# Kernel optimization log

Measured on AMD Instinct MI355X. Metric: run time of the kernel, lower is better.

## Reference

```python
import jax, jax.numpy as jnp
import numpy as np

BASE_RES = 192          # image_shape = [192, 192]
VIEWS = 128             # radial views
READOUT_OS = 2.0        # readout oversampling
SAMPLES = int(BASE_RES * READOUT_OS)  # 384 samples per spoke


def _radial_traj_and_weights():
    """Linear-ordered full-range 2D radial trajectory + ramp density weights."""
    t = jnp.arange(SAMPLES, dtype=jnp.float32)
    # radius spans [-pi, pi) along each spoke (NUFFT convention)
    r = (t - SAMPLES / 2) / (SAMPLES / 2) * jnp.pi            # [samples]
    theta = jnp.arange(VIEWS, dtype=jnp.float32) * (jnp.pi / VIEWS)  # [views]
    kx = r[None, :] * jnp.cos(theta)[:, None]                 # [views, samples]
    ky = r[None, :] * jnp.sin(theta)[:, None]
    points = jnp.stack([kx, ky], axis=-1).reshape(-1, 2)      # [M, 2]
    # geometric (ramp) density compensation: weight ~ |k| with DC floor
    rho = jnp.abs(r) / jnp.pi                                 # [samples], in [0, 1]
    w = jnp.maximum(rho, 1.0 / SAMPLES)                       # avoid zero at DC
    weights = jnp.broadcast_to(w[None, :], (VIEWS, SAMPLES)).reshape(-1)  # [M]
    return points, weights


def setup_inputs() -> dict:
    key = jax.random.key(0)
    x = jax.random.normal(key, (2, BASE_RES, BASE_RES, 2), dtype=jnp.float32)
    points, weights = _radial_traj_and_weights()
    return {"x": x, "points": points, "weights": weights}


def _nudft_resample(xc, points, weights):
    """Type-2 NUDFT (forward) -> density comp -> type-1 NUDFT (adjoint).

    xc: complex [C, B, H, W]; points: [M, 2] in [-pi, pi); weights: [M].
    The 2D nonuniform DFT phase factorizes per axis: exp(-i(kx*nx + ky*ny)).
    """
    C, B, H, W = xc.shape
    nx = (jnp.arange(H, dtype=jnp.float32) - H // 2)          # grid indices
    ny = (jnp.arange(W, dtype=jnp.float32) - W // 2)
    Ax = jnp.exp(-1j * (points[:, 0:1] * nx[None, :]).astype(jnp.complex64))  # [M, H]
    Ay = jnp.exp(-1j * (points[:, 1:2] * ny[None, :]).astype(jnp.complex64))  # [M, W]
    # type-2: k[m] = sum_{h,w} x[h,w] exp(-i(kx_m h + ky_m w))
    tmp = jnp.einsum('cbhw,mh->cbmw', xc, Ax)                 # [C, B, M, W]
    k = jnp.einsum('cbmw,mw->cbm', tmp, Ay)                   # [C, B, M]
    # density compensation
    k = k * weights.astype(jnp.complex64)
    # type-1 adjoint: img[h,w] = sum_m k[m] exp(+i(kx_m h + ky_m w))
    tmp2 = jnp.einsum('cbm,mh->cbmh', k, jnp.conj(Ax))        # [C, B, M, H]
    img = jnp.einsum('cbmh,mw->cbhw', tmp2, jnp.conj(Ay))     # [C, B, H, W]
    # scale by 1 / num_elements(image_shape)
    return img / jnp.asarray(H * W, dtype=jnp.complex64)


def reference(x, points, weights):
    # inputs [B, H, W, C] -> channels-first [C, B, H, W] (layer's perm)
    rank = x.ndim
    perm = [rank - 1] + list(range(rank - 1))
    xc = jnp.transpose(x, perm).astype(jnp.complex64)
    img = _nudft_resample(xc, points, weights)
    out = jnp.abs(img)                                        # layer dtype is real
    inv_perm = list(range(1, rank)) + [0]
    return jnp.transpose(out, inv_perm)                       # [B, H, W, C]
```

## Files before the change

kernel.cpp:

```cpp
#include <hip/hip_runtime.h>
#include <math.h>


#define HH 192
#define WW 192
#define NVIEWS 128
#define NSAMP 384
#define NPIX (HH*WW)
#define HALFT 193
#define M2 12545
#define M2P 12672
#define KTOT 25344
#define NSPLITK 33

typedef __attribute__((ext_vector_type(8))) short bf16x8;
typedef __attribute__((ext_vector_type(4))) float f32x4;
typedef __attribute__((ext_vector_type(8))) unsigned short u16x8;

__device__ __forceinline__ void rot(float& cr, float& ci, float dr, float di) {
  float nr = cr*dr - ci*di;
  float ni = cr*di + ci*dr;
  cr = nr; ci = ni;
}
__device__ __forceinline__ unsigned short f2b(float f) {
  unsigned int u = __float_as_uint(f);
  u += 0x7fffu + ((u >> 16) & 1u);
  return (unsigned short)(u >> 16);
}
__device__ __forceinline__ float b2f(unsigned short h) {
  return __uint_as_float(((unsigned int)h) << 16);
}

__global__ __launch_bounds__(256) void phase_kernel(
    const float* __restrict__ points, const float* __restrict__ x,
    unsigned short* __restrict__ BT, unsigned short* __restrict__ CxT,
    unsigned short* __restrict__ SxT, unsigned short* __restrict__ Am,
    unsigned short* __restrict__ XT) {
  const int v2 = blockIdx.x;
  const int role = blockIdx.y;
  const int t = threadIdx.x;
  if (role == 8) {
    for (int idx = v2*256 + t; idx < 768*192; idx += 65*256) {
      const int n = idx / 192, h = idx - n*192;
      const int cb = n / 192, w = n - cb*192;
      const int b = cb >> 1, c = cb & 1;
      XT[idx] = f2b(x[(((size_t)b*HH + h)*WW + w)*2 + c]);
    }
    return;
  }
  if (t >= HALFT) return;
  if (role < 4) {
    const int hsplit = role;
    const float kx = points[(v2*NSAMP + t)*2 + 0];
    const int m2 = v2*HALFT + t;
    const int h0 = hsplit*48;
    float cr, ci; __sincosf(kx*(float)(h0-96), &ci, &cr);
    float dr, di; __sincosf(kx, &di, &dr);
    u16x8 pc, ps;
    for (int j = 0; j < 48; ++j) {
      const int h = h0 + j;
      CxT[(size_t)h*M2P + m2] = f2b(cr);
      SxT[(size_t)h*M2P + m2] = f2b(ci);
      pc[j&7] = f2b(cr); ps[j&7] = f2b(ci);
      if ((j&7) == 7) {
        *(u16x8*)(Am + (size_t)m2*192 + (h-7))         = pc;
        *(u16x8*)(Am + (size_t)(12672+m2)*192 + (h-7)) = ps;
      }
      rot(cr, ci, dr, di);
    }
  } else {
    const int wsplit = role - 4;
    const float ky = points[(v2*NSAMP + t)*2 + 1];
    const int kap = v2*HALFT + t;
    const int w0 = wsplit*48;
    float cr, ci; __sincosf(ky*(float)(w0-96), &ci, &cr);
    float dr, di; __sincosf(ky, &di, &dr);
    for (int j = 0; j < 48; ++j) {
      BT[(size_t)(w0+j)*KTOT + kap]       = f2b(cr);
      BT[(size_t)(w0+j)*KTOT + M2P + kap] = f2b(ci);
      rot(cr, ci, dr, di);
    }
  }
}


__global__ __launch_bounds__(256) void gemm1_kernel(
    const unsigned short* __restrict__ Am, const unsigned short* __restrict__ XT,
    const float* __restrict__ points, float* __restrict__ Abuf) {
  __shared__ float lds[2][128][2];
  const int L = blockIdx.x;
  const int idx0 = (L & 7)*99 + (L >> 3);
  const int mt = idx0 >> 2;
  const int cb = idx0 & 3;
  const int wv = threadIdx.x >> 6;
  const int lane = threadIdx.x & 63;
  const int r = lane & 15, kg = lane >> 4;
  const int mhalf = wv >> 1;
  const int whalf = wv & 1;
  const int mbase = mt*128 + mhalf*64;
  const int wbase = whalf*96;
  const int nbase = cb*192 + wbase;

  f32x4 acc[4][6];
  #pragma unroll
  for (int a = 0; a < 4; ++a)
    #pragma unroll
    for (int b = 0; b < 6; ++b) acc[a][b] = (f32x4){0.f,0.f,0.f,0.f};

  const unsigned short* Ap = Am + (size_t)(mbase + r)*192 + kg*8;
  const unsigned short* Bp = XT + (size_t)(nbase + r)*192 + kg*8;
  #pragma unroll
  for (int ks = 0; ks < 6; ++ks) {
    bf16x8 af[4], bfr[6];
    #pragma unroll
    for (int mf = 0; mf < 4; ++mf)
      af[mf] = *(const bf16x8*)(Ap + (size_t)mf*16*192 + ks*32);
    #pragma unroll
    for (int nf = 0; nf < 6; ++nf)
      bfr[nf] = *(const bf16x8*)(Bp + (size_t)nf*16*192 + ks*32);
    #pragma unroll
    for (int mf = 0; mf < 4; ++mf)
      #pragma unroll
      for (int nf = 0; nf < 6; ++nf)
        acc[mf][nf] = __builtin_amdgcn_mfma_f32_16x16x32_bf16(
            af[mf], bfr[nf], acc[mf][nf], 0, 0, 0);
  }

  const bool isCx = (mt < 99);
  const int m2w = mbase - (isCx ? 0 : 12672);
  float accA[16], accB[16];
  #pragma unroll
  for (int mf = 0; mf < 4; ++mf)
    #pragma unroll
    for (int reg = 0; reg < 4; ++reg) {
      const int m2 = m2w + mf*16 + kg*4 + reg;
      const int v2 = m2 / HALFT, t = m2 - v2*HALFT;
      const float ky = points[(v2*NSAMP + t)*2 + 1];
      float a0 = 0.f, b0 = 0.f;
      #pragma unroll
      for (int nf = 0; nf < 6; ++nf) {
        const float wo = (float)(wbase + nf*16 + r - 96);
        float sy, cy; __sincosf(ky*wo, &sy, &cy);
        const float g = acc[mf][nf][reg];
        a0 = fmaf(g, cy, a0);
        b0 = fmaf(g, sy, b0);
      }
      accA[mf*4+reg] = a0; accB[mf*4+reg] = b0;
    }
  #pragma unroll
  for (int msk = 1; msk <= 8; msk <<= 1) {
    #pragma unroll
    for (int i = 0; i < 16; ++i) {
      accA[i] += __shfl_xor(accA[i], msk);
      accB[i] += __shfl_xor(accB[i], msk);
    }
  }
  if (r == 0) {
    #pragma unroll
    for (int mf = 0; mf < 4; ++mf)
      #pragma unroll
      for (int reg = 0; reg < 4; ++reg) {
        const int mloc = mhalf*64 + mf*16 + kg*4 + reg;
        lds[whalf][mloc][0] = accA[mf*4+reg];
        lds[whalf][mloc][1] = accB[mf*4+reg];
      }
  }
  __syncthreads();
  {
    const int tid = threadIdx.x;
    const int mloc = tid >> 1, slot = tid & 1;
    const float val = lds[0][mloc][slot] + lds[1][mloc][slot];
    const int m2 = mt*128 + mloc - (isCx ? 0 : 12672);
    const int oidx = isCx ? (slot ? 3 : 0) : (slot ? 1 : 2);
    Abuf[((size_t)cb*M2P + m2)*4 + oidx] = val;
  }
}

__global__ __launch_bounds__(256) void combine2_kernel(
    const float* __restrict__ Abuf, const float* __restrict__ weights,
    float* __restrict__ combos, float* __restrict__ K2edge) {
  const int m2 = blockIdx.x*256 + threadIdx.x;
  if (m2 >= M2P) return;
  if (m2 >= M2) {
    #pragma unroll
    for (int q = 0; q < 16; ++q) combos[(size_t)q*M2P + m2] = 0.f;
    return;
  }
  const int v2 = m2 / HALFT, t = m2 - v2*HALFT;
  float f = weights[t] * (1.0f/36864.0f);
  if (t != 0 && t != 192) f *= 2.0f;
  const bool hp = (v2 >= 1 && v2 <= 63);
  #pragma unroll
  for (int cb = 0; cb < 4; ++cb) {
    const float4 A = *(const float4*)(Abuf + ((size_t)cb*M2P + m2)*4);
    const float A1 = A.x, A2 = A.y, A3 = A.z, A4 = A.w;
    float p0, p1, q0, q1;
    if (hp) {
      p0 = 2.f*f*A1; p1 = 2.f*f*A3; q0 = 2.f*f*A4; q1 = 2.f*f*A2;
    } else {
      const float kr = f*(A1 - A2), ki = -f*(A3 + A4);
      p0 = kr; p1 = -ki; q0 = -ki; q1 = -kr;
    }
    combos[(size_t)(cb*4+0)*M2P + m2] = p0;
    combos[(size_t)(cb*4+1)*M2P + m2] = p1;
    combos[(size_t)(cb*4+2)*M2P + m2] = q0;
    combos[(size_t)(cb*4+3)*M2P + m2] = q1;
    if (t == 0 || t == 192) {
      const int d = (t == 0) ? 0 : 1;
      float* e = K2edge + ((v2*2 + d)*4 + cb)*2;
      e[0] = f*(A1 - A2); e[1] = -f*(A3 + A4);
      if (hp) {
        float* e2 = K2edge + (((128 - v2)*2 + d)*4 + cb)*2;
        e2[0] = f*(A1 + A2); e2[1] = f*(A3 - A4);
      }
    }
  }
}


__global__ __launch_bounds__(256) void tmat_kernel(
    const float* __restrict__ combos, const unsigned short* __restrict__ CxT,
    const unsigned short* __restrict__ SxT, unsigned short* __restrict__ A) {
  const int m2 = blockIdx.x*256 + threadIdx.x;
  if (m2 >= M2P) return;
  const int h = blockIdx.y;
  const float cx = b2f(CxT[(size_t)h*M2P + m2]);
  const float sx = b2f(SxT[(size_t)h*M2P + m2]);
  #pragma unroll
  for (int cb = 0; cb < 4; ++cb) {
    unsigned short* Arow = A + (size_t)(cb*192 + h)*KTOT;
    const float p0 = combos[(size_t)(cb*4+0)*M2P + m2];
    const float p1 = combos[(size_t)(cb*4+1)*M2P + m2];
    const float q0 = combos[(size_t)(cb*4+2)*M2P + m2];
    const float q1 = combos[(size_t)(cb*4+3)*M2P + m2];
    Arow[m2]       = f2b(p0*cx + p1*sx);
    Arow[M2P + m2] = f2b(q0*cx + q1*sx);
  }
}

__global__ __launch_bounds__(256) void adj_gemm(
    const unsigned short* __restrict__ A, const unsigned short* __restrict__ BT,
    float* __restrict__ partials) {
  const int L = blockIdx.x;
  const int xcd = L & 7, slot = L >> 3;
  const int g = slot / 6;
  const int kc = g*8 + xcd;
  if (kc >= NSPLITK) return;
  const int mt = slot - g*6;
  const int wv = threadIdx.x >> 6;
  const int lane = threadIdx.x & 63;
  const int r = lane & 15, kg = lane >> 4;
  const int jbase = mt*128 + (wv>>1)*64;
  const int wbase = (wv&1)*96;
  const int kb = kc*768 + kg*8;

  f32x4 acc[4][6];
  #pragma unroll
  for (int a = 0; a < 4; ++a)
    #pragma unroll
    for (int b = 0; b < 6; ++b) acc[a][b] = (f32x4){0.f,0.f,0.f,0.f};

  const unsigned short* Ap = A + (size_t)(jbase + r)*KTOT + kb;
  const unsigned short* Bp = BT + (size_t)(wbase + r)*KTOT + kb;
  for (int ks = 0; ks < 24; ++ks) {
    bf16x8 af[4], bfr[6];
    #pragma unroll
    for (int mf = 0; mf < 4; ++mf)
      af[mf] = *(const bf16x8*)(Ap + (size_t)mf*16*KTOT + ks*32);
    #pragma unroll
    for (int nf = 0; nf < 6; ++nf)
      bfr[nf] = *(const bf16x8*)(Bp + (size_t)nf*16*KTOT + ks*32);
    #pragma unroll
    for (int mf = 0; mf < 4; ++mf)
      #pragma unroll
      for (int nf = 0; nf < 6; ++nf)
        acc[mf][nf] = __builtin_amdgcn_mfma_f32_16x16x32_bf16(
            af[mf], bfr[nf], acc[mf][nf], 0, 0, 0);
  }
  float* base = partials + (size_t)kc*192*768;
  #pragma unroll
  for (int mf = 0; mf < 4; ++mf)
    #pragma unroll
    for (int nf = 0; nf < 6; ++nf) {
      const int w = wbase + nf*16 + r;
      const int j = jbase + mf*16 + kg*4;
      *(f32x4*)(base + (size_t)w*768 + j) = acc[mf][nf];
    }
}

__global__ __launch_bounds__(256) void finish_kernel(
    const unsigned short* __restrict__ BT, const unsigned short* __restrict__ CxT,
    const unsigned short* __restrict__ SxT, const float* __restrict__ K2edge,
    const float* __restrict__ partials, float* __restrict__ out) {
  __shared__ float cxs[65][8], sxs[65][8], cys[65][8], sys[65][8];
  __shared__ float redI[4][64][4], redR[4][64][4];
  const int bx = blockIdx.x;
  const int h0 = (bx/24)*8, w0 = (bx%24)*8;
  const int tid = threadIdx.x;
  for (int i = tid; i < 65*8; i += 256) {
    const int v2 = i >> 3, e = i & 7;
    const int kap = v2*HALFT;
    cxs[v2][e] = b2f(CxT[(size_t)(h0+e)*M2P + kap]);
    sxs[v2][e] = b2f(SxT[(size_t)(h0+e)*M2P + kap]);
    cys[v2][e] = b2f(BT[(size_t)(w0+e)*KTOT + kap]);
    sys[v2][e] = b2f(BT[(size_t)(w0+e)*KTOT + M2P + kap]);
  }
  __syncthreads();
  const int g = tid >> 6, hi = (tid >> 3) & 7, wi = tid & 7;
  const int h = h0 + hi, w = w0 + wi;
  float im[4] = {0,0,0,0};
  for (int v = g*32; v < g*32 + 32; ++v) {
    const int v2 = (v <= 64) ? v : 128 - v;
    const float sg = (v <= 64) ? 1.f : -1.f;
    const float cx = cxs[v2][hi], sx = sg*sxs[v2][hi];
    const float cy = cys[v2][wi], sy = sys[v2][wi];
    const float t1 = cx*sy + sx*cy;
    const float t2 = cx*cy - sx*sy;
    const int idx = v*16;
    #pragma unroll
    for (int cb = 0; cb < 4; ++cb)
      im[cb] += K2edge[idx + cb*2]*t1 + K2edge[idx + cb*2 + 1]*t2;
  }
  float re[4] = {0,0,0,0};
  for (int kc = g; kc < NSPLITK; kc += 4) {
    const float* p = partials + (size_t)kc*147456 + (size_t)w*768;
    #pragma unroll
    for (int cb = 0; cb < 4; ++cb)
      re[cb] += p[cb*192 + h];
  }
  const int p = tid & 63;
  #pragma unroll
  for (int cb = 0; cb < 4; ++cb) { redI[g][p][cb] = im[cb]; redR[g][p][cb] = re[cb]; }
  __syncthreads();
  if (g == 0) {
    #pragma unroll
    for (int cb = 0; cb < 4; ++cb) {
      im[cb] += redI[1][p][cb] + redI[2][p][cb] + redI[3][p][cb];
      re[cb] += redR[1][p][cb] + redR[2][p][cb] + redR[3][p][cb];
    }
    const int pix = h*192 + w;
    #pragma unroll
    for (int b = 0; b < 2; ++b)
      #pragma unroll
      for (int c = 0; c < 2; ++c) {
        const int cb = b*2 + c;
        out[((size_t)b*NPIX + pix)*2 + c] = sqrtf(re[cb]*re[cb] + im[cb]*im[cb]);
      }
  }
}


template <int HPER>
__global__ __launch_bounds__(192) void fwd_kernel(
    const float* __restrict__ x, const float* __restrict__ points,
    float* __restrict__ kpart) {
  const int v = blockIdx.x;
  const int split = blockIdx.y;
  const int t = threadIdx.x;
  const int m = v*NSAMP + t;
  const float kx = points[2*m+0];
  const float ky = points[2*m+1];
  const int h0 = split*HPER;

  float kr[4] = {0,0,0,0}, ki[4] = {0,0,0,0};
  float cyr, cyi; __sincosf(96.0f*ky, &cyi, &cyr);
  float dyr, dyi; __sincosf(-ky, &dyi, &dyr);
  float cx0r, cx0i; __sincosf(kx*(float)(96-h0), &cx0i, &cx0r);
  float dxr, dxi; __sincosf(-kx, &dxi, &dxr);

  for (int wp = 0; wp < 96; ++wp) {
    const int w0 = wp*2;
    float g0r[4]={0,0,0,0}, g0i[4]={0,0,0,0};
    float g1r[4]={0,0,0,0}, g1i[4]={0,0,0,0};
    float cxr = cx0r, cxi = cx0i;
    const float* p0 = x + (h0*WW + w0)*2;
    const float* p1 = p0 + HH*WW*2;
    #pragma unroll 4
    for (int h = 0; h < HPER; ++h) {
      float4 a = *(const float4*)(p0 + h*(WW*2));
      float4 b = *(const float4*)(p1 + h*(WW*2));
      g0r[0] += a.x*cxr; g0i[0] += a.x*cxi;
      g0r[1] += a.y*cxr; g0i[1] += a.y*cxi;
      g1r[0] += a.z*cxr; g1i[0] += a.z*cxi;
      g1r[1] += a.w*cxr; g1i[1] += a.w*cxi;
      g0r[2] += b.x*cxr; g0i[2] += b.x*cxi;
      g0r[3] += b.y*cxr; g0i[3] += b.y*cxi;
      g1r[2] += b.z*cxr; g1i[2] += b.z*cxi;
      g1r[3] += b.w*cxr; g1i[3] += b.w*cxi;
      rot(cxr, cxi, dxr, dxi);
    }
    #pragma unroll
    for (int cb = 0; cb < 4; ++cb) {
      kr[cb] += g0r[cb]*cyr - g0i[cb]*cyi;
      ki[cb] += g0r[cb]*cyi + g0i[cb]*cyr;
    }
    rot(cyr, cyi, dyr, dyi);
    #pragma unroll
    for (int cb = 0; cb < 4; ++cb) {
      kr[cb] += g1r[cb]*cyr - g1i[cb]*cyi;
      ki[cb] += g1r[cb]*cyi + g1i[cb]*cyr;
    }
    rot(cyr, cyi, dyr, dyi);
  }
  float* o = kpart + (((split*NVIEWS + v)*192 + t)*4)*2;
  #pragma unroll
  for (int cb = 0; cb < 4; ++cb) { o[2*cb] = kr[cb]; o[2*cb+1] = ki[cb]; }
}

__global__ __launch_bounds__(256) void dc_kernel(
    const float* __restrict__ x, float* __restrict__ dcsum) {
  const int tid = threadIdx.x;
  float s0=0.f, s1=0.f, s2=0.f, s3=0.f;
  for (int i = tid; i < NPIX; i += 256) {
    float2 a = *(const float2*)(x + i*2);
    float2 b = *(const float2*)(x + HH*WW*2 + i*2);
    s0 += a.x; s1 += a.y; s2 += b.x; s3 += b.y;
  }
  #pragma unroll
  for (int off = 32; off > 0; off >>= 1) {
    s0 += __shfl_down(s0, off);
    s1 += __shfl_down(s1, off);
    s2 += __shfl_down(s2, off);
    s3 += __shfl_down(s3, off);
  }
  __shared__ float red[4][4];
  const int wv = tid >> 6, ln = tid & 63;
  if (ln == 0) { red[0][wv]=s0; red[1][wv]=s1; red[2][wv]=s2; red[3][wv]=s3; }
  __syncthreads();
  if (tid < 4) {
    float tot = red[tid][0]+red[tid][1]+red[tid][2]+red[tid][3];
    dcsum[2*tid] = tot; dcsum[2*tid+1] = 0.0f;
  }
}

__global__ __launch_bounds__(256) void combine_kernel(
    const float* __restrict__ kpart, const float* __restrict__ dcsum,
    const float* __restrict__ weights, float* __restrict__ K2, int nsplit) {
  const int idx = blockIdx.x*256 + threadIdx.x;
  if (idx >= NVIEWS*HALFT) return;
  const int v = idx / HALFT, t = idx % HALFT;
  float f = weights[t] * (1.0f/36864.0f);
  if (t != 0 && t != 192) f *= 2.0f;
  float o[8];
  if (t == 192) {
    #pragma unroll
    for (int cb = 0; cb < 4; ++cb) { o[2*cb] = f*dcsum[2*cb]; o[2*cb+1] = f*dcsum[2*cb+1]; }
  } else {
    #pragma unroll
    for (int cb = 0; cb < 4; ++cb) {
      float ar = 0.f, ai = 0.f;
      for (int s = 0; s < nsplit; ++s) {
        const float* p = kpart + (((s*NVIEWS + v)*192 + t)*4 + cb)*2;
        ar += p[0]; ai += p[1];
      }
      o[2*cb] = f*ar; o[2*cb+1] = f*ai;
    }
  }
  float* q = K2 + idx*8;
  #pragma unroll
  for (int j = 0; j < 8; ++j) q[j] = o[j];
}

template <int VPC>
__global__ __launch_bounds__(256) void adj_kernel(
    const float* __restrict__ K2, const float* __restrict__ points,
    float* __restrict__ imgpart) {
  const int pix = blockIdx.x*256 + threadIdx.x;
  const int chunk = blockIdx.y;
  const float nh = (float)(pix / WW - 96);
  const float nw = (float)(pix % WW - 96);
  float re[4] = {0,0,0,0}, im[4] = {0,0,0,0};
  const float INVPI = 0.3183098861837907f;
  const float PI192 = 3.14159265358979f / 192.0f;
  for (int v = chunk*VPC; v < chunk*VPC + VPC; ++v) {
    const float ct = -points[2*(v*NSAMP)+0] * INVPI;
    const float st = -points[2*(v*NSAMP)+1] * INVPI;
    const float alpha = ct*nh + st*nw;
    const float delta = alpha * PI192;
    float dr, di; __sincosf(delta, &di, &dr);
    float c0r, c0i; __sincosf(-192.0f*delta, &c0i, &c0r);
    const float* Kv = K2 + v*HALFT*8;
    #pragma unroll
    for (int cb = 0; cb < 4; ++cb) {
      float a = Kv[2*cb], b = Kv[2*cb+1];
      re[cb] += a*c0r - b*c0i;
      im[cb] += a*c0i + b*c0r;
    }
    float d2r = dr*dr - di*di, d2i = 2.0f*dr*di;
    float ar = c0r*dr - c0i*di, ai = c0r*di + c0i*dr;
    float br = ar*dr - ai*di,  bi = ar*di + ai*dr;
    for (int i = 0; i < 95; ++i) {
      const float* ka = Kv + (2*i+1)*8;
      const float* kb = Kv + (2*i+2)*8;
      #pragma unroll
      for (int cb = 0; cb < 4; ++cb)
        re[cb] += ka[2*cb]*ar - ka[2*cb+1]*ai;
      #pragma unroll
      for (int cb = 0; cb < 4; ++cb)
        re[cb] += kb[2*cb]*br - kb[2*cb+1]*bi;
      rot(ar, ai, d2r, d2i);
      rot(br, bi, d2r, d2i);
    }
    {
      const float* ka = Kv + 191*8;
      #pragma unroll
      for (int cb = 0; cb < 4; ++cb)
        re[cb] += ka[2*cb]*ar - ka[2*cb+1]*ai;
    }
    const float* kd = Kv + 192*8;
    #pragma unroll
    for (int cb = 0; cb < 4; ++cb) { re[cb] += kd[2*cb]; im[cb] += kd[2*cb+1]; }
  }
  float* o = imgpart + (chunk*NPIX + pix)*8;
  #pragma unroll
  for (int cb = 0; cb < 4; ++cb) { o[2*cb] = re[cb]; o[2*cb+1] = im[cb]; }
}

__global__ __launch_bounds__(256) void out_fb_kernel(
    const float* __restrict__ imgpart, float* __restrict__ out, int nchunk) {
  const int pix = blockIdx.x*256 + threadIdx.x;
  float re[4] = {0,0,0,0}, im[4] = {0,0,0,0};
  for (int ch = 0; ch < nchunk; ++ch) {
    const float* p = imgpart + (ch*NPIX + pix)*8;
    #pragma unroll
    for (int cb = 0; cb < 4; ++cb) { re[cb] += p[2*cb]; im[cb] += p[2*cb+1]; }
  }
  #pragma unroll
  for (int b = 0; b < 2; ++b)
    #pragma unroll
    for (int c = 0; c < 2; ++c) {
      const int cb = b*2 + c;
      out[(b*NPIX + pix)*2 + c] = sqrtf(re[cb]*re[cb] + im[cb]*im[cb]);
    }
}

extern "C" void kernel_launch(void* const* d_in, const int* in_sizes, int n_in,
                              void* d_out, int out_size, void* d_ws, size_t ws_size,
                              hipStream_t stream) {
  const float* x       = (const float*)d_in[0];
  const float* points  = (const float*)d_in[1];
  const float* weights = (const float*)d_in[2];
  float* out = (float*)d_out;

  const size_t NEED = 79265792ull;
  if (ws_size >= NEED) {
    char* wsb = (char*)d_ws;
    unsigned short* BT   = (unsigned short*)(wsb + 0);
    unsigned short* CxT  = (unsigned short*)(wsb + 9732096);
    unsigned short* SxT  = (unsigned short*)(wsb + 14598144);
    float* combos        = (float*)(wsb + 19464192);
    float* K2edge        = (float*)(wsb + 20275200);
    char* S              = wsb + 20283392;
    unsigned short* Am   = (unsigned short*)(S + 0);
    unsigned short* XT   = (unsigned short*)(S + 9732096);
    float* Abuf          = (float*)(S + 10027008);
    unsigned short* Aadj = (unsigned short*)(S + 0);
    float* partials      = (float*)(S + 38928384);

    phase_kernel<<<dim3(65,9), 256, 0, stream>>>(points, x, BT, CxT, SxT, Am, XT);
    gemm1_kernel<<<792, 256, 0, stream>>>(Am, XT, points, Abuf);
    combine2_kernel<<<(M2P + 255)/256, 256, 0, stream>>>(
        Abuf, weights, combos, K2edge);
    tmat_kernel<<<dim3((M2P + 255)/256, 192), 256, 0, stream>>>(
        combos, CxT, SxT, Aadj);
    adj_gemm<<<240, 256, 0, stream>>>(Aadj, BT, partials);
    finish_kernel<<<576, 256, 0, stream>>>(BT, CxT, SxT, K2edge, partials, out);
  } else {
    float* ws = (float*)d_ws;
    const size_t ws_floats = ws_size / sizeof(float);
    int nsplit = 16, nchunk = 16;
    auto need = [&](int ns, int nc) -> size_t {
      return (size_t)ns*196608 + 8 + 197632 + (size_t)nc*294912;
    };
    while (need(nsplit, nchunk) > ws_floats && nchunk > 1) nchunk >>= 1;
    while (need(nsplit, nchunk) > ws_floats && nsplit > 1) nsplit >>= 1;

    float* kpart   = ws;
    float* dcsum   = kpart + (size_t)nsplit*196608;
    float* K2      = dcsum + 8;
    float* imgpart = K2 + 197632;

    switch (nsplit) {
      case 16: fwd_kernel<12><<<dim3(NVIEWS,16), 192, 0, stream>>>(x, points, kpart); break;
      case 8:  fwd_kernel<24><<<dim3(NVIEWS,8),  192, 0, stream>>>(x, points, kpart); break;
      case 4:  fwd_kernel<48><<<dim3(NVIEWS,4),  192, 0, stream>>>(x, points, kpart); break;
      case 2:  fwd_kernel<96><<<dim3(NVIEWS,2),  192, 0, stream>>>(x, points, kpart); break;
      default: fwd_kernel<192><<<dim3(NVIEWS,1), 192, 0, stream>>>(x, points, kpart); break;
    }
    dc_kernel<<<1, 256, 0, stream>>>(x, dcsum);
    combine_kernel<<<(NVIEWS*HALFT + 255)/256, 256, 0, stream>>>(
        kpart, dcsum, weights, K2, nsplit);
    switch (nchunk) {
      case 16: adj_kernel<8>  <<<dim3(NPIX/256,16), 256, 0, stream>>>(K2, points, imgpart); break;
      case 8:  adj_kernel<16> <<<dim3(NPIX/256,8),  256, 0, stream>>>(K2, points, imgpart); break;
      case 4:  adj_kernel<32> <<<dim3(NPIX/256,4),  256, 0, stream>>>(K2, points, imgpart); break;
      case 2:  adj_kernel<64> <<<dim3(NPIX/256,2),  256, 0, stream>>>(K2, points, imgpart); break;
      default: adj_kernel<128><<<dim3(NPIX/256,1),  256, 0, stream>>>(K2, points, imgpart); break;
    }
    out_fb_kernel<<<NPIX/256, 256, 0, stream>>>(imgpart, out, nchunk);
  }
}
```

Measured before the change: 126.4 us.

## Split gemm1 over W halves and double adj_gemm split-K for more blocks

gemm1 now splits the W dimension across two blocks, writing two partial Abuf copies that combine2 sums, which doubles the block count and halves per-wave accumulators. A precomputed ky vector replaces the per-element division and points gather in the gemm1 epilogue. adj_gemm becomes templated on K steps, and with enough workspace it uses 66 K-splits of half length instead of 33 to fill more CUs. In exchange it writes more partials and makes finish_kernel reduce twice as many of them.

```diff
diff --git a/kernel.cpp b/kernel.cpp
--- a/kernel.cpp
+++ b/kernel.cpp
@@ -11,7 +11,7 @@
 #define M2 12545
 #define M2P 12672
 #define KTOT 25344
-#define NSPLITK 33
+#define ABUF_STRIDE 202752
 
 typedef __attribute__((ext_vector_type(8))) short bf16x8;
 typedef __attribute__((ext_vector_type(4))) float f32x4;
@@ -35,7 +35,7 @@
     const float* __restrict__ points, const float* __restrict__ x,
     unsigned short* __restrict__ BT, unsigned short* __restrict__ CxT,
     unsigned short* __restrict__ SxT, unsigned short* __restrict__ Am,
-    unsigned short* __restrict__ XT) {
+    unsigned short* __restrict__ XT, float* __restrict__ kyv) {
   const int v2 = blockIdx.x;
   const int role = blockIdx.y;
   const int t = threadIdx.x;
@@ -45,6 +45,14 @@
       const int cb = n / 192, w = n - cb*192;
       const int b = cb >> 1, c = cb & 1;
       XT[idx] = f2b(x[(((size_t)b*HH + h)*WW + w)*2 + c]);
+    }
+    for (int idx = v2*256 + t; idx < M2P; idx += 65*256) {
+      if (idx < M2) {
+        const int v2b = idx / HALFT, tb = idx - v2b*HALFT;
+        kyv[idx] = points[(v2b*NSAMP + tb)*2 + 1];
+      } else {
+        kyv[idx] = 0.f;
+      }
     }
     return;
   }
@@ -86,42 +94,44 @@
 
 __global__ __launch_bounds__(256) void gemm1_kernel(
     const unsigned short* __restrict__ Am, const unsigned short* __restrict__ XT,
-    const float* __restrict__ points, float* __restrict__ Abuf) {
+    const float* __restrict__ kyv, float* __restrict__ Abuf2) {
   __shared__ float lds[2][128][2];
   const int L = blockIdx.x;
-  const int idx0 = (L & 7)*99 + (L >> 3);
-  const int mt = idx0 >> 2;
-  const int cb = idx0 & 3;
+  const int xcd = L & 7, s = L >> 3;
+  const int mt = xcd*25 + (s >> 3);
+  if (mt >= 198) return;
+  const int cbwp = s & 7;
+  const int cb = cbwp >> 1, wp = cbwp & 1;
   const int wv = threadIdx.x >> 6;
   const int lane = threadIdx.x & 63;
   const int r = lane & 15, kg = lane >> 4;
   const int mhalf = wv >> 1;
-  const int whalf = wv & 1;
+  const int wq = wv & 1;
   const int mbase = mt*128 + mhalf*64;
-  const int wbase = whalf*96;
+  const int wbase = wp*96 + wq*48;
   const int nbase = cb*192 + wbase;
 
-  f32x4 acc[4][6];
+  f32x4 acc[4][3];
   #pragma unroll
   for (int a = 0; a < 4; ++a)
     #pragma unroll
-    for (int b = 0; b < 6; ++b) acc[a][b] = (f32x4){0.f,0.f,0.f,0.f};
+    for (int b = 0; b < 3; ++b) acc[a][b] = (f32x4){0.f,0.f,0.f,0.f};
 
   const unsigned short* Ap = Am + (size_t)(mbase + r)*192 + kg*8;
   const unsigned short* Bp = XT + (size_t)(nbase + r)*192 + kg*8;
   #pragma unroll
   for (int ks = 0; ks < 6; ++ks) {
-    bf16x8 af[4], bfr[6];
+    bf16x8 af[4], bfr[3];
     #pragma unroll
     for (int mf = 0; mf < 4; ++mf)
       af[mf] = *(const bf16x8*)(Ap + (size_t)mf*16*192 + ks*32);
     #pragma unroll
-    for (int nf = 0; nf < 6; ++nf)
+    for (int nf = 0; nf < 3; ++nf)
       bfr[nf] = *(const bf16x8*)(Bp + (size_t)nf*16*192 + ks*32);
     #pragma unroll
     for (int mf = 0; mf < 4; ++mf)
       #pragma unroll
-      for (int nf = 0; nf < 6; ++nf)
+      for (int nf = 0; nf < 3; ++nf)
         acc[mf][nf] = __builtin_amdgcn_mfma_f32_16x16x32_bf16(
             af[mf], bfr[nf], acc[mf][nf], 0, 0, 0);
   }
@@ -134,11 +144,10 @@
     #pragma unroll
     for (int reg = 0; reg < 4; ++reg) {
       const int m2 = m2w + mf*16 + kg*4 + reg;
-      const int v2 = m2 / HALFT, t = m2 - v2*HALFT;
-      const float ky = points[(v2*NSAMP + t)*2 + 1];
+      const float ky = kyv[m2];
       float a0 = 0.f, b0 = 0.f;
       #pragma unroll
-      for (int nf = 0; nf < 6; ++nf) {
+      for (int nf = 0; nf < 3; ++nf) {
         const float wo = (float)(wbase + nf*16 + r - 96);
         float sy, cy; __sincosf(ky*wo, &sy, &cy);
         const float g = acc[mf][nf][reg];
@@ -161,8 +170,8 @@
       #pragma unroll
       for (int reg = 0; reg < 4; ++reg) {
         const int mloc = mhalf*64 + mf*16 + kg*4 + reg;
-        lds[whalf][mloc][0] = accA[mf*4+reg];
-        lds[whalf][mloc][1] = accB[mf*4+reg];
+        lds[wq][mloc][0] = accA[mf*4+reg];
+        lds[wq][mloc][1] = accB[mf*4+reg];
       }
   }
   __syncthreads();
@@ -172,12 +181,12 @@
     const float val = lds[0][mloc][slot] + lds[1][mloc][slot];
     const int m2 = mt*128 + mloc - (isCx ? 0 : 12672);
     const int oidx = isCx ? (slot ? 3 : 0) : (slot ? 1 : 2);
-    Abuf[((size_t)cb*M2P + m2)*4 + oidx] = val;
+    Abuf2[(size_t)wp*ABUF_STRIDE + ((size_t)cb*M2P + m2)*4 + oidx] = val;
   }
 }
 
 __global__ __launch_bounds__(256) void combine2_kernel(
-    const float* __restrict__ Abuf, const float* __restrict__ weights,
+    const float* __restrict__ Abuf2, const float* __restrict__ weights,
     float* __restrict__ combos, float* __restrict__ K2edge) {
   const int m2 = blockIdx.x*256 + threadIdx.x;
   if (m2 >= M2P) return;
@@ -192,8 +201,10 @@
   const bool hp = (v2 >= 1 && v2 <= 63);
   #pragma unroll
   for (int cb = 0; cb < 4; ++cb) {
-    const float4 A = *(const float4*)(Abuf + ((size_t)cb*M2P + m2)*4);
-    const float A1 = A.x, A2 = A.y, A3 = A.z, A4 = A.w;
+    const float4 Aa = *(const float4*)(Abuf2 + ((size_t)cb*M2P + m2)*4);
+    const float4 Ab = *(const float4*)(Abuf2 + ABUF_STRIDE + ((size_t)cb*M2P + m2)*4);
+    const float A1 = Aa.x + Ab.x, A2 = Aa.y + Ab.y;
+    const float A3 = Aa.z + Ab.z, A4 = Aa.w + Ab.w;
     float p0, p1, q0, q1;
     if (hp) {
       p0 = 2.f*f*A1; p1 = 2.f*f*A3; q0 = 2.f*f*A4; q1 = 2.f*f*A2;
@@ -238,21 +249,22 @@
   }
 }
 
+template <int KSTEPS>
 __global__ __launch_bounds__(256) void adj_gemm(
     const unsigned short* __restrict__ A, const unsigned short* __restrict__ BT,
-    float* __restrict__ partials) {
+    float* __restrict__ partials, int nsplit) {
   const int L = blockIdx.x;
   const int xcd = L & 7, slot = L >> 3;
   const int g = slot / 6;
   const int kc = g*8 + xcd;
-  if (kc >= NSPLITK) return;
+  if (kc >= nsplit) return;
   const int mt = slot - g*6;
   const int wv = threadIdx.x >> 6;
   const int lane = threadIdx.x & 63;
   const int r = lane & 15, kg = lane >> 4;
   const int jbase = mt*128 + (wv>>1)*64;
   const int wbase = (wv&1)*96;
-  const int kb = kc*768 + kg*8;
+  const int kb = kc*(KSTEPS*32) + kg*8;
 
   f32x4 acc[4][6];
   #pragma unroll
@@ -262,7 +274,7 @@
 
   const unsigned short* Ap = A + (size_t)(jbase + r)*KTOT + kb;
   const unsigned short* Bp = BT + (size_t)(wbase + r)*KTOT + kb;
-  for (int ks = 0; ks < 24; ++ks) {
+  for (int ks = 0; ks < KSTEPS; ++ks) {
     bf16x8 af[4], bfr[6];
     #pragma unroll
     for (int mf = 0; mf < 4; ++mf)
@@ -291,7 +303,7 @@
 __global__ __launch_bounds__(256) void finish_kernel(
     const unsigned short* __restrict__ BT, const unsigned short* __restrict__ CxT,
     const unsigned short* __restrict__ SxT, const float* __restrict__ K2edge,
-    const float* __restrict__ partials, float* __restrict__ out) {
+    const float* __restrict__ partials, float* __restrict__ out, int nsplit) {
   __shared__ float cxs[65][8], sxs[65][8], cys[65][8], sys[65][8];
   __shared__ float redI[4][64][4], redR[4][64][4];
   const int bx = blockIdx.x;
@@ -322,7 +334,7 @@
       im[cb] += K2edge[idx + cb*2]*t1 + K2edge[idx + cb*2 + 1]*t2;
   }
   float re[4] = {0,0,0,0};
-  for (int kc = g; kc < NSPLITK; kc += 4) {
+  for (int kc = g; kc < nsplit; kc += 4) {
     const float* p = partials + (size_t)kc*147456 + (size_t)w*768;
     #pragma unroll
     for (int cb = 0; cb < 4; ++cb)
@@ -542,29 +554,39 @@
   const float* weights = (const float*)d_in[2];
   float* out = (float*)d_out;
 
-  const size_t NEED = 79265792ull;
-  if (ws_size >= NEED) {
+  const size_t OFF_S   = 20334080ull;
+  const size_t SZ_AADJ = 38928384ull;
+  const size_t NEED66  = OFF_S + SZ_AADJ + 66ull*589824;
+  const size_t NEED33  = OFF_S + SZ_AADJ + 33ull*589824;
+
+  if (ws_size >= NEED33) {
+    const int nsplit = (ws_size >= NEED66) ? 66 : 33;
     char* wsb = (char*)d_ws;
     unsigned short* BT   = (unsigned short*)(wsb + 0);
     unsigned short* CxT  = (unsigned short*)(wsb + 9732096);
     unsigned short* SxT  = (unsigned short*)(wsb + 14598144);
     float* combos        = (float*)(wsb + 19464192);
     float* K2edge        = (float*)(wsb + 20275200);
-    char* S              = wsb + 20283392;
+    float* kyv           = (float*)(wsb + 20283392);
+    char* S              = wsb + OFF_S;
     unsigned short* Am   = (unsigned short*)(S + 0);
     unsigned short* XT   = (unsigned short*)(S + 9732096);
-    float* Abuf          = (float*)(S + 10027008);
+    float* Abuf2         = (float*)(S + 10027008);
     unsigned short* Aadj = (unsigned short*)(S + 0);
-    float* partials      = (float*)(S + 38928384);
-
-    phase_kernel<<<dim3(65,9), 256, 0, stream>>>(points, x, BT, CxT, SxT, Am, XT);
-    gemm1_kernel<<<792, 256, 0, stream>>>(Am, XT, points, Abuf);
+    float* partials      = (float*)(S + SZ_AADJ);
+
+    phase_kernel<<<dim3(65,9), 256, 0, stream>>>(points, x, BT, CxT, SxT, Am, XT, kyv);
+    gemm1_kernel<<<1600, 256, 0, stream>>>(Am, XT, kyv, Abuf2);
     combine2_kernel<<<(M2P + 255)/256, 256, 0, stream>>>(
-        Abuf, weights, combos, K2edge);
+        Abuf2, weights, combos, K2edge);
     tmat_kernel<<<dim3((M2P + 255)/256, 192), 256, 0, stream>>>(
         combos, CxT, SxT, Aadj);
-    adj_gemm<<<240, 256, 0, stream>>>(Aadj, BT, partials);
-    finish_kernel<<<576, 256, 0, stream>>>(BT, CxT, SxT, K2edge, partials, out);
+    if (nsplit == 66) {
+      adj_gemm<12><<<8*9*6, 256, 0, stream>>>(Aadj, BT, partials, 66);
+    } else {
+      adj_gemm<24><<<8*5*6, 256, 0, stream>>>(Aadj, BT, partials, 33);
+    }
+    finish_kernel<<<576, 256, 0, stream>>>(BT, CxT, SxT, K2edge, partials, out, nsplit);
   } else {
     float* ws = (float*)d_ws;
     const size_t ws_floats = ws_size / sizeof(float);
```

Result: slower. 134.6 us (+6.5%).
